# Performance work log

Hardware: AMD Instinct MI355X
Metric: run time of the kernel (lower is better)

Reference implementation:

```python
import jax, jax.numpy as jnp
import numpy as np

N = 10000       # nodes (= number of eigenpairs)
NFEAT = 512
NCLASS = 64     # hidden size of attention/FFN when norm='none'
HID = 128       # feat_encoder hidden
DIM = 32        # eig encoder hidden_dim
K = 10          # outer loop count of ParamNonHarmonicEncoding
NF = DIM // 2   # num_freq = 16
OMEGA = 50.0
DMIN = 0.25
NLAYER = 1


def _ln(x, g, b, eps=1e-5):
    m = jnp.mean(x, axis=-1, keepdims=True)
    v = jnp.mean((x - m) ** 2, axis=-1, keepdims=True)
    return g * (x - m) / jnp.sqrt(v + eps) + b


def setup_inputs() -> dict:
    key = jax.random.key(0)
    ks = jax.random.split(key, 32)
    f32 = jnp.float32
    def w(k, shape, s=0.05):
        return jax.random.normal(k, shape, dtype=f32) * s
    inp = {
        "e": jax.random.uniform(ks[0], (N,), dtype=f32),
        "u": jax.random.normal(ks[1], (N, N), dtype=f32) / np.float32(np.sqrt(N)),
        "x": jax.random.normal(ks[2], (N, NFEAT), dtype=f32),
        # feat_encoder: Linear(nfeat,hid) -> ReLU -> Linear(hid,nclass)
        "fe_w1": w(ks[3], (NFEAT, HID)), "fe_b1": jnp.zeros((HID,), f32),
        "fe_w2": w(ks[4], (HID, NCLASS)), "fe_b2": jnp.zeros((NCLASS,), f32),
        # ParamNonHarmonicEncoding
        "freq_deltas": jax.random.uniform(ks[5], (NF,), dtype=f32) * 0.5,
        "freq_bias": jnp.zeros((), f32),
        "readout_w": w(ks[6], (K, 1 + 2 * NF), 0.1),
        "readout_b": jnp.zeros((K,), f32),
        "alpha_w": w(ks[7], (K, 1), 0.3),   # nn.Linear(k,1,bias=False)
        # mha pre-norm
        "mha_ln_g": jnp.ones((NCLASS,), f32), "mha_ln_b": jnp.zeros((NCLASS,), f32),
        # Diff attention (H=1, hidden=nclass)
        "wq1": w(ks[8], (NCLASS, NCLASS)), "bq1": jnp.zeros((NCLASS,), f32),
        "wk1": w(ks[9], (NCLASS, NCLASS)), "bk1": jnp.zeros((NCLASS,), f32),
        "wq2": w(ks[10], (NCLASS, NCLASS)), "bq2": jnp.zeros((NCLASS,), f32),
        "wk2": w(ks[11], (NCLASS, NCLASS)), "bk2": jnp.zeros((NCLASS,), f32),
        "wv": w(ks[12], (NCLASS, NCLASS)), "bv": jnp.zeros((NCLASS,), f32),
        "lq1": w(ks[13], (NCLASS,), 0.1), "lk1": w(ks[14], (NCLASS,), 0.1),
        "lq2": w(ks[15], (NCLASS,), 0.1), "lk2": w(ks[16], (NCLASS,), 0.1),
        "attn_ln_g": jnp.ones((NCLASS,), f32), "attn_ln_b": jnp.zeros((NCLASS,), f32),
        "out_w": w(ks[17], (NCLASS, NCLASS)), "out_b": jnp.zeros((NCLASS,), f32),
        # gating
        "gate_ln_g": jnp.ones((3 * NCLASS,), f32), "gate_ln_b": jnp.zeros((3 * NCLASS,), f32),
        "gate_w": w(ks[18], (3 * NCLASS, 3)), "gate_b": jnp.zeros((3,), f32),
        # FFN
        "ffn_ln_g": jnp.ones((NCLASS,), f32), "ffn_ln_b": jnp.zeros((NCLASS,), f32),
        "ffn_w1": w(ks[19], (NCLASS, NCLASS)), "ffn_b1": jnp.zeros((NCLASS,), f32),
        "ffn_w2": w(ks[20], (NCLASS, NCLASS)), "ffn_b2": jnp.zeros((NCLASS,), f32),
    }
    return inp


def reference(e, u, x, fe_w1, fe_b1, fe_w2, fe_b2,
              freq_deltas, freq_bias, readout_w, readout_b, alpha_w,
              mha_ln_g, mha_ln_b,
              wq1, bq1, wk1, bk1, wq2, bq2, wk2, bk2, wv, bv,
              lq1, lk1, lq2, lk2, attn_ln_g, attn_ln_b, out_w, out_b,
              gate_ln_g, gate_ln_b, gate_w, gate_b,
              ffn_ln_g, ffn_ln_b, ffn_w1, ffn_b1, ffn_w2, ffn_b2):
    # feat encoder (all dropouts are 0 / eval mode)
    h = jnp.maximum(x @ fe_w1 + fe_b1, 0.0) @ fe_w2 + fe_b2          # [N, C]

    # ParamNonHarmonicEncoding, vectorized over the k powers
    deltas = jax.nn.softplus(freq_deltas) + DMIN
    freqs = jnp.cumsum(deltas) + freq_bias
    freqs = OMEGA * jnp.tanh(freqs / OMEGA)                           # [F]
    powers = e[:, None] ** jnp.arange(1, K + 1, dtype=e.dtype)        # [N, K]
    phase = powers[:, :, None] * freqs                                # [N, K, F]
    ns = jnp.asarray(NF ** 0.5, e.dtype)
    feat = jnp.concatenate(
        [jnp.ones_like(powers)[..., None], jnp.sin(phase) / ns, jnp.cos(phase) / ns],
        axis=-1)                                                      # [N, K, 1+2F]
    eig = jnp.einsum('nkf,kf->nk', feat, readout_w) + readout_b      # [N, K]
    new_e = eig @ alpha_w                                             # [N, 1]

    for layer in range(NLAYER):
        # spectral propagation: u @ diag-like(new_e) @ u^T @ h
        utx = u.T @ h                                                 # [N, C]
        h_fur = u @ (new_e * utx)                                     # [N, C]

        # differential linear attention
        mh = _ln(h, mha_ln_g, mha_ln_b)
        q1 = mh @ wq1 + bq1; k1 = mh @ wk1 + bk1
        q2 = mh @ wq2 + bq2; k2 = mh @ wk2 + bk2
        v = mh @ wv + bv
        k1v = k1.T @ v                                                # [C, C]
        k2v = k2.T @ v
        lam1 = jnp.exp(jnp.sum(lq1 * lk1))
        lam2 = jnp.exp(jnp.sum(lq2 * lk2))
        lam_init = 0.8 - 0.6 * float(np.exp(-0.3 * layer))
        lam_full = lam1 - lam2 + lam_init
        xa = q1 @ k1v - (q2 @ k2v) * lam_full
        xa = _ln(xa, attn_ln_g, attn_ln_b) * (1.0 - lam_init)
        mha_h = xa @ out_w + out_b                                    # [N, C]

        # gated mixing
        cat = jnp.concatenate([h, mha_h, h_fur], axis=-1)             # [N, 3C]
        g = jax.nn.softmax(_ln(cat, gate_ln_g, gate_ln_b) @ gate_w + gate_b, axis=-1)
        mix = h * g[:, 0:1] + mha_h * g[:, 1:2] + h_fur * g[:, 2:3]

        f = _ln(mix, ffn_ln_g, ffn_ln_b)
        f = jax.nn.gelu(f @ ffn_w1 + ffn_b1, approximate=False) @ ffn_w2 + ffn_b2
        h = mix + f
    return h
```

## Files before the change

kernel.cpp:

```cpp
#include <hip/hip_runtime.h>
#include <hip/hip_bf16.h>
#include <math.h>

#define NN 10000
#define J48 10048
#define CHUNKS 157
#define CPS 20
#define SPLITS 8

typedef __bf16 bf16;
typedef bf16 bf16x8 __attribute__((ext_vector_type(8)));
typedef float f32x4 __attribute__((ext_vector_type(4)));

#define SYNC_LDS() do {                                      \
    asm volatile("s_waitcnt lgkmcnt(0)" ::: "memory");       \
    __builtin_amdgcn_sched_barrier(0);                       \
    __builtin_amdgcn_s_barrier();                            \
    __builtin_amdgcn_sched_barrier(0);                       \
  } while (0)

__device__ __forceinline__ float wave_sum64(float v) {
#pragma unroll
  for (int m = 32; m >= 1; m >>= 1) v += __shfl_xor(v, m, 64);
  return v;
}

__global__ void prep_kernel(const float* __restrict__ w1, const float* __restrict__ w2,
                            const float* __restrict__ wq1, const float* __restrict__ wk1,
                            const float* __restrict__ wq2, const float* __restrict__ wk2,
                            const float* __restrict__ wvw,
                            const float* __restrict__ bq1, const float* __restrict__ bk1,
                            const float* __restrict__ bq2, const float* __restrict__ bk2,
                            const float* __restrict__ bvv,
                            const float* __restrict__ lq1, const float* __restrict__ lk1,
                            const float* __restrict__ lq2, const float* __restrict__ lk2,
                            const float* __restrict__ freq_deltas, const float* __restrict__ freq_bias,
                            bf16* __restrict__ w1T, bf16* __restrict__ w2T, bf16* __restrict__ qkvT,
                            float* __restrict__ bqkv, float* __restrict__ freqs, float* __restrict__ lamb) {
  int tid = blockIdx.x * blockDim.x + threadIdx.x;
  int nthr = gridDim.x * blockDim.x;
  for (int i = tid; i < 512 * 128; i += nthr) {
    int o = i >> 9, k = i & 511;
    w1T[i] = (bf16)w1[k * 128 + o];
  }
  for (int i = tid; i < 64 * 128; i += nthr) {
    int o = i >> 7, k = i & 127;
    w2T[i] = (bf16)w2[k * 64 + o];
  }
  for (int i = tid; i < 320 * 64; i += nthr) {
    int r = i >> 6, k = i & 63;
    const float* W = (r < 64) ? wq1 : (r < 128) ? wk1 : (r < 192) ? wq2 : (r < 256) ? wk2 : wvw;
    qkvT[i] = (bf16)W[k * 64 + (r & 63)];
  }
  for (int i = tid; i < 320; i += nthr) {
    const float* B = (i < 64) ? bq1 : (i < 128) ? bk1 : (i < 192) ? bq2 : (i < 256) ? bk2 : bvv;
    bqkv[i] = B[i & 63];
  }
  if (blockIdx.x == 0) {
    if (threadIdx.x == 0) {
      float acc = freq_bias[0];
      for (int f = 0; f < 16; f++) {
        acc += log1pf(expf(freq_deltas[f])) + 0.25f;
        freqs[f] = 50.0f * tanhf(acc * (1.0f / 50.0f));
      }
    }
    if (threadIdx.x >= 64 && threadIdx.x < 128) {
      int l = threadIdx.x - 64;
      float s1 = wave_sum64(lq1[l] * lk1[l]);
      float s2 = wave_sum64(lq2[l] * lk2[l]);
      if (l == 0) lamb[0] = expf(s1) - expf(s2) + 0.2f;
    }
  }
}

__global__ void newe_kernel(const float* __restrict__ e, const float* __restrict__ rw,
                            const float* __restrict__ rb, const float* __restrict__ aw,
                            const float* __restrict__ freqs, float* __restrict__ newe) {
  int n = blockIdx.x * blockDim.x + threadIdx.x;
  if (n >= NN) return;
  float fr[16];
#pragma unroll
  for (int f = 0; f < 16; f++) fr[f] = freqs[f];
  float ev = e[n], p = 1.0f, acc = 0.0f;
  for (int k = 0; k < 10; k++) {
    p *= ev;
    float s = rb[k] + rw[k * 33];
#pragma unroll
    for (int f = 0; f < 16; f++) {
      float ph = p * fr[f];
      s += 0.25f * (__sinf(ph) * rw[k * 33 + 1 + f] + __cosf(ph) * rw[k * 33 + 17 + f]);
    }
    acc += s * aw[k];
  }
  newe[n] = acc;
}

__global__ __launch_bounds__(256) void g1_kernel(const float* __restrict__ x, const bf16* __restrict__ w1T,
                                                 const float* __restrict__ b1, bf16* __restrict__ t1b) {
  __shared__ bf16 la[64][40];
  __shared__ bf16 lb[128][40];
  const int bm = blockIdx.x * 64;
  const int lane = threadIdx.x & 63, wvid = threadIdx.x >> 6;
// ... 138 lines not shown
    uint4 val = make_uint4(0u, 0u, 0u, 0u);
    if (row < NN) val = *(const uint4*)(mh + (size_t)row * 64 + seg);
    *(uint4*)&la[m][seg] = val;
  }
#pragma unroll
  for (int r = 0; r < 10; r++) {
    int slot = threadIdx.x * 10 + r;
    int n = slot >> 3, seg = (slot & 7) * 8;
    *(uint4*)&lb[n][seg] = *(const uint4*)(qkvT + n * 64 + seg);
  }
  __syncthreads();
  f32x4 acc[20] = {};
#pragma unroll
  for (int ks = 0; ks < 2; ks++) {
    bf16x8 af = *(const bf16x8*)&la[wvid * 16 + (lane & 15)][ks * 32 + (lane >> 4) * 8];
#pragma unroll
    for (int s = 0; s < 20; s++) {
      bf16x8 bfr = *(const bf16x8*)&lb[s * 16 + (lane & 15)][ks * 32 + (lane >> 4) * 8];
      acc[s] = __builtin_amdgcn_mfma_f32_16x16x32_bf16(af, bfr, acc[s], 0, 0, 0);
    }
  }
#pragma unroll
  for (int s = 0; s < 20; s++) {
    int col = s * 16 + (lane & 15);
    float bvv = bqkv[col];
    bf16* dst; int dc, stride;
    if (col < 64)       { dst = qq; dc = col;       stride = 128; }
    else if (col < 128) { dst = kv; dc = col - 64;  stride = 192; }
    else if (col < 192) { dst = qq; dc = col - 64;  stride = 128; }
    else                { dst = kv; dc = col - 128; stride = 192; }
#pragma unroll
    for (int r = 0; r < 4; r++) {
      int row = bm + wvid * 16 + (lane >> 4) * 4 + r;
      if (row < NN) dst[(size_t)row * stride + dc] = (bf16)(acc[s][r] + bvv);
    }
  }
}

__global__ __launch_bounds__(256) void r1_kernel(const bf16* __restrict__ kv, float* __restrict__ part) {
  int b = blockIdx.x;
  int c1 = threadIdx.x & 63, grp = threadIdx.x >> 6;
  int r0 = b * 16;
  float a1[16] = {}, a2[16] = {};
  for (int r = 0; r < 16; r++) {
    const bf16* rowp = kv + (size_t)(r0 + r) * 192;
    float k1 = (float)rowp[c1];
    float k2 = (float)rowp[64 + c1];
    union { uint4 v; bf16 b[8]; } v0, v1;
    v0.v = *(const uint4*)(rowp + 128 + grp * 16);
    v1.v = *(const uint4*)(rowp + 136 + grp * 16);
#pragma unroll
    for (int q = 0; q < 8; q++) {
      float va = (float)v0.b[q], vb = (float)v1.b[q];
      a1[q] += k1 * va; a2[q] += k2 * va;
      a1[8 + q] += k1 * vb; a2[8 + q] += k2 * vb;
    }
  }
  float* p1 = part + (size_t)b * 8192 + (size_t)c1 * 64 + grp * 16;
  float* p2 = p1 + 4096;
#pragma unroll
  for (int q = 0; q < 16; q++) { p1[q] = a1[q]; p2[q] = a2[q]; }
}

__global__ __launch_bounds__(256) void r2a_kernel(const float* __restrict__ part, float* __restrict__ part2) {
  int flat = blockIdx.x * 256 + threadIdx.x;
  int y = blockIdx.y;
  int b0 = y * 79, b1 = min(625, b0 + 79);
  float s = 0.f;
  for (int b = b0; b < b1; b++) s += part[(size_t)b * 8192 + flat];
  part2[(size_t)flat * 8 + y] = s;
}

__global__ void r2b_kernel(const float* __restrict__ part2, const float* __restrict__ lamb, bf16* __restrict__ Bt) {
  int flat = blockIdx.x * 256 + threadIdx.x;
  int mat = flat >> 12, rem = flat & 4095;
  int d = rem >> 6, c = rem & 63;
  f32x4 lo = *(const f32x4*)(part2 + (size_t)flat * 8);
  f32x4 hi = *(const f32x4*)(part2 + (size_t)flat * 8 + 4);
  float s = lo[0] + lo[1] + lo[2] + lo[3] + hi[0] + hi[1] + hi[2] + hi[3];
  float v = mat ? (-lamb[0] * s) : s;
  Bt[c * 128 + mat * 64 + d] = (bf16)v;
}

__global__ __launch_bounds__(256) void d_split_kernel(const float* __restrict__ u, const bf16* __restrict__ hT,
                                                      float* __restrict__ dpart) {
  __shared__ bf16 la[64][72];
  __shared__ bf16 lb[64][72];
  const int j0 = blockIdx.x * 64;
  const int sk = blockIdx.y;
  const int c0 = sk * CPS, c1e = min(CHUNKS, c0 + CPS);
  const int t = threadIdx.x;
  const int lane = t & 63, wv = t >> 6;
  const int jl = (t & 15) * 4;
  const int ir = (t >> 4) * 4;
  f32x4 acc[4] = {};
  uint4 aC[2];
  float4 bC[4];
  auto fetchAll = [&](int i0) {
#pragma unroll
    for (int r = 0; r < 2; r++) {
      int slot = t * 2 + r;
      int c = slot >> 3, seg = (slot & 7) * 8;
      int i = i0 + seg;
      if (i + 7 < NN) aC[r] = *(const uint4*)(hT + (size_t)c * NN + i);
      else {
        union { uint4 v; bf16 b[8]; } tu;
#pragma unroll
        for (int q = 0; q < 8; q++) tu.b[q] = (i + q < NN) ? hT[(size_t)c * NN + i + q] : (bf16)0.f;
        aC[r] = tu.v;
      }
    }
#pragma unroll
    for (int q = 0; q < 4; q++) {
      int i = i0 + ir + q;
      if (i < NN && (j0 + jl + 3) < NN) bC[q] = *(const float4*)(u + (size_t)i * NN + j0 + jl);
      else if (i < NN) {
        float tmp[4];
#pragma unroll
        for (int q2 = 0; q2 < 4; q2++) tmp[q2] = (j0 + jl + q2 < NN) ? u[(size_t)i * NN + j0 + jl + q2] : 0.f;
        bC[q] = make_float4(tmp[0], tmp[1], tmp[2], tmp[3]);
      } else bC[q] = make_float4(0.f, 0.f, 0.f, 0.f);
    }
  };
  auto storeAll = [&]() {
#pragma unroll
    for (int r = 0; r < 2; r++) {
      int slot = t * 2 + r;
      int c = slot >> 3, seg = (slot & 7) * 8;
      *(uint4*)&la[c][seg] = aC[r];
    }
#pragma unroll
    for (int q2 = 0; q2 < 4; q2++) {
      int j = jl + q2;
      int isw = ir ^ (((j >> 2) & 3) << 3);
      union { uint2 w; bf16 b[4]; } pk;
      pk.b[0] = (bf16)((float*)&bC[0])[q2];
      pk.b[1] = (bf16)((float*)&bC[1])[q2];
      pk.b[2] = (bf16)((float*)&bC[2])[q2];
      pk.b[3] = (bf16)((float*)&bC[3])[q2];
      *(uint2*)&lb[j][isw] = pk.w;
    }
  };
  fetchAll(c0 * 64);
  for (int ch = c0; ch < c1e; ch++) {
    storeAll();
    if (ch + 1 < c1e) fetchAll((ch + 1) * 64);
    SYNC_LDS();
#pragma unroll
    for (int ks = 0; ks < 2; ks++) {
      bf16x8 af = *(const bf16x8*)&la[wv * 16 + (lane & 15)][ks * 32 + (lane >> 4) * 8];
#pragma unroll
      for (int s = 0; s < 4; s++) {
        int j = s * 16 + (lane & 15);
        int ioff = (ks * 32 + (lane >> 4) * 8) ^ (((j >> 2) & 3) << 3);
        bf16x8 bfr = *(const bf16x8*)&lb[j][ioff];
        acc[s] = __builtin_amdgcn_mfma_f32_16x16x32_bf16(af, bfr, acc[s], 0, 0, 0);
      }
    }
    SYNC_LDS();
  }
#pragma unroll
  for (int s = 0; s < 4; s++) {
    int j = j0 + s * 16 + (lane & 15);
#pragma unroll
    for (int r = 0; r < 4; r++) {
      int c = wv * 16 + (lane >> 4) * 4 + r;
      dpart[((size_t)sk * 64 + c) * J48 + j] = acc[s][r];
    }
  }
}

__global__ void dred_kernel(const float* __restrict__ dpart, const float* __restrict__ newe,
                            bf16* __restrict__ wutxT) {
  int idx = blockIdx.x * 256 + threadIdx.x;
  int c = idx / 2512;
  int j = (idx - c * 2512) * 4;
  if (c >= 64 || j >= NN) return;
  f32x4 s = {};
  for (int sk = 0; sk < SPLITS; sk++)
    s += *(const f32x4*)(dpart + ((size_t)sk * 64 + c) * J48 + j);
  union { uint2 w; bf16 b[4]; } pk;
#pragma unroll
  for (int q = 0; q < 4; q++) pk.b[q] = (bf16)(newe[j + q] * s[q]);
  *(uint2*)&wutxT[(size_t)c * NN + j] = pk.w;
}

__global__ __launch_bounds__(256) void e_split_kernel(const float* __restrict__ u, const bf16* __restrict__ wutxT,
                                                      float* __restrict__ epart) {
  __shared__ bf16 la[64][72];
  __shared__ bf16 lb[64][72];
  const int bm = blockIdx.x * 64;
  const int sk = blockIdx.y;
  const int c0 = sk * CPS, c1e = min(CHUNKS, c0 + CPS);
  const int t = threadIdx.x;
  const int lane = t & 63, wv = t >> 6;
  const int mA = t >> 2, segA = (t & 3) * 16;
  const int mrow = bm + mA;
  f32x4 acc[4] = {};
  float4 aC[4];
  uint4 bC[2];
  auto fetchAll = [&](int j0) {
    int j = j0 + segA;
    if (mrow < NN && j + 15 < NN) {
      const float4* p = (const float4*)(u + (size_t)mrow * NN + j);
      aC[0] = p[0]; aC[1] = p[1]; aC[2] = p[2]; aC[3] = p[3];
    } else {
#pragma unroll
      for (int q = 0; q < 4; q++) {
        float tmp[4];
#pragma unroll
        for (int q2 = 0; q2 < 4; q2++) {
          int jj = j + q * 4 + q2;
          tmp[q2] = (mrow < NN && jj < NN) ? u[(size_t)mrow * NN + jj] : 0.f;
        }
        aC[q] = make_float4(tmp[0], tmp[1], tmp[2], tmp[3]);
      }
    }
#pragma unroll
    for (int r = 0; r < 2; r++) {
      int slot = t * 2 + r;
      int c = slot >> 3, seg = (slot & 7) * 8;
      int jj = j0 + seg;
      if (jj + 7 < NN) bC[r] = *(const uint4*)(wutxT + (size_t)c * NN + jj);
      else {
        union { uint4 v; bf16 b[8]; } tu;
#pragma unroll
        for (int q = 0; q < 8; q++) tu.b[q] = (jj + q < NN) ? wutxT[(size_t)c * NN + jj + q] : (bf16)0.f;
        bC[r] = tu.v;
      }
    }
  };
  auto storeAll = [&]() {
    union { uint4 v[2]; bf16 b[16]; } pk;
#pragma unroll
    for (int q = 0; q < 4; q++)
#pragma unroll
      for (int q2 = 0; q2 < 4; q2++) pk.b[q * 4 + q2] = (bf16)((float*)&aC[q])[q2];
    *(uint4*)&la[mA][segA] = pk.v[0];
    *(uint4*)&la[mA][segA + 8] = pk.v[1];
#pragma unroll
    for (int r = 0; r < 2; r++) {
      int slot = t * 2 + r;
      int c = slot >> 3, seg = (slot & 7) * 8;
      *(uint4*)&lb[c][seg] = bC[r];
    }
  };
  fetchAll(c0 * 64);
  for (int ch = c0; ch < c1e; ch++) {
    storeAll();
    if (ch + 1 < c1e) fetchAll((ch + 1) * 64);
    SYNC_LDS();
#pragma unroll
    for (int ks = 0; ks < 2; ks++) {
      bf16x8 af = *(const bf16x8*)&la[wv * 16 + (lane & 15)][ks * 32 + (lane >> 4) * 8];
#pragma unroll
      for (int s = 0; s < 4; s++) {
        bf16x8 bfr = *(const bf16x8*)&lb[s * 16 + (lane & 15)][ks * 32 + (lane >> 4) * 8];
        acc[s] = __builtin_amdgcn_mfma_f32_16x16x32_bf16(af, bfr, acc[s], 0, 0, 0);
      }
    }
    SYNC_LDS();
  }
#pragma unroll
  for (int s = 0; s < 4; s++) {
    int col = s * 16 + (lane & 15);
#pragma unroll
    for (int r = 0; r < 4; r++) {
      int row = wv * 16 + (lane >> 4) * 4 + r;
      epart[((size_t)sk * J48 + bm + row) * 64 + col] = acc[s][r];
    }
  }
}

__global__ void ered_kernel(const float* __restrict__ epart, float* __restrict__ h_fur) {
  int idx = blockIdx.x * 256 + threadIdx.x;
  if (idx >= NN * 16) return;
  size_t off = (size_t)idx * 4;
  f32x4 s = {};
  for (int sk = 0; sk < SPLITS; sk++)
    s += *(const f32x4*)(epart + (size_t)sk * (J48 * 64) + off);
  *(f32x4*)(h_fur + off) = s;
}

__global__ __launch_bounds__(256) void hattn_kernel(const bf16* __restrict__ qq, const bf16* __restrict__ Bt,
                                                    const float* __restrict__ g, const float* __restrict__ b,
                                                    bf16* __restrict__ xan) {
  __shared__ bf16 la[64][136];
  __shared__ bf16 lb[64][136];
  const int bm = blockIdx.x * 64;
  const int lane = threadIdx.x & 63, wvid = threadIdx.x >> 6;
#pragma unroll
  for (int r = 0; r < 4; r++) {
    int slot = threadIdx.x * 4 + r;
    int m = slot >> 4, seg = (slot & 15) * 8;
    int row = bm + m;
    uint4 val = make_uint4(0u, 0u, 0u, 0u);
    if (row < NN) val = *(const uint4*)(qq + (size_t)row * 128 + seg);
    *(uint4*)&la[m][seg] = val;
    *(uint4*)&lb[m][seg] = *(const uint4*)(Bt + m * 128 + seg);
  }
  __syncthreads();
  f32x4 acc[4] = {};
#pragma unroll
  for (int ks = 0; ks < 4; ks++) {
    bf16x8 af = *(const bf16x8*)&la[wvid * 16 + (lane & 15)][ks * 32 + (lane >> 4) * 8];
#pragma unroll
    for (int s = 0; s < 4; s++) {
      bf16x8 bfr = *(const bf16x8*)&lb[s * 16 + (lane & 15)][ks * 32 + (lane >> 4) * 8];
      acc[s] = __builtin_amdgcn_mfma_f32_16x16x32_bf16(af, bfr, acc[s], 0, 0, 0);
    }
  }
#pragma unroll
  for (int r = 0; r < 4; r++) {
    float psum = acc[0][r] + acc[1][r] + acc[2][r] + acc[3][r];
#pragma unroll
    for (int msk = 1; msk < 16; msk <<= 1) psum += __shfl_xor(psum, msk, 64);
    float mean = psum * (1.0f / 64.0f);
    float pvar = 0.f;
#pragma unroll
    for (int s = 0; s < 4; s++) { float dd = acc[s][r] - mean; pvar += dd * dd; }
#pragma unroll
    for (int msk = 1; msk < 16; msk <<= 1) pvar += __shfl_xor(pvar, msk, 64);
    float rsq = rsqrtf(pvar * (1.0f / 64.0f) + 1e-5f);
    int row = bm + wvid * 16 + (lane >> 4) * 4 + r;
    if (row < NN) {
#pragma unroll
      for (int s = 0; s < 4; s++) {
        int col = s * 16 + (lane & 15);
        float o = 0.8f * (g[col] * (acc[s][r] - mean) * rsq + b[col]);
        xan[(size_t)row * 64 + col] = (bf16)o;
      }
    }
  }
}

__global__ __launch_bounds__(256) void final_kernel(const float* __restrict__ h, const float* __restrict__ h_fur,
                                                    const bf16* __restrict__ xan,
                                                    const float* __restrict__ out_w, const float* __restrict__ out_b,
                                                    const float* __restrict__ gg, const float* __restrict__ gb,
                                                    const float* __restrict__ gw, const float* __restrict__ gbias,
                                                    const float* __restrict__ fg, const float* __restrict__ fb,
                                                    const float* __restrict__ fw1, const float* __restrict__ fb1,
                                                    const float* __restrict__ fw2, const float* __restrict__ fb2,
                                                    float* __restrict__ out) {
  __shared__ float s_ow[64][64];
  __shared__ float s_w1[64][64];
  __shared__ float s_w2[64][64];
  __shared__ float s_gw[192][3];
  __shared__ float s_row[4][64];
  const int lane = threadIdx.x & 63, wvid = threadIdx.x >> 6;
  for (int i = threadIdx.x; i < 4096; i += 256) {
    ((float*)s_ow)[i] = out_w[i];
    ((float*)s_w1)[i] = fw1[i];
    ((float*)s_w2)[i] = fw2[i];
  }
  for (int i = threadIdx.x; i < 576; i += 256) ((float*)s_gw)[i] = gw[i];
  const int row = blockIdx.x * 4 + wvid;
  float x_h = h[(size_t)row * 64 + lane];
  float x_f = h_fur[(size_t)row * 64 + lane];
  float x_a = (float)xan[(size_t)row * 64 + lane];
  s_row[wvid][lane] = x_a;
  __syncthreads();
  float mha = out_b[lane];
#pragma unroll 8
  for (int d = 0; d < 64; d++) mha += s_row[wvid][d] * s_ow[d][lane];
  float m3 = wave_sum64(x_h + mha + x_f) * (1.0f / 192.0f);
  float dh = x_h - m3, dm = mha - m3, df = x_f - m3;
  float v3 = wave_sum64(dh * dh + dm * dm + df * df) * (1.0f / 192.0f);
  float rs3 = rsqrtf(v3 + 1e-5f);
  float l0 = gg[lane] * dh * rs3 + gb[lane];
  float l1 = gg[64 + lane] * dm * rs3 + gb[64 + lane];
  float l2 = gg[128 + lane] * df * rs3 + gb[128 + lane];
  float p0 = l0 * s_gw[lane][0] + l1 * s_gw[64 + lane][0] + l2 * s_gw[128 + lane][0];
  float p1 = l0 * s_gw[lane][1] + l1 * s_gw[64 + lane][1] + l2 * s_gw[128 + lane][1];
  float p2 = l0 * s_gw[lane][2] + l1 * s_gw[64 + lane][2] + l2 * s_gw[128 + lane][2];
  p0 = wave_sum64(p0) + gbias[0];
  p1 = wave_sum64(p1) + gbias[1];
  p2 = wave_sum64(p2) + gbias[2];
  float mx = fmaxf(p0, fmaxf(p1, p2));
  float e0 = expf(p0 - mx), e1 = expf(p1 - mx), e2 = expf(p2 - mx);
  float inv = 1.0f / (e0 + e1 + e2);
  float mix = x_h * (e0 * inv) + mha * (e1 * inv) + x_f * (e2 * inv);
  float mf = wave_sum64(mix) * (1.0f / 64.0f);
  float dmx = mix - mf;
  float vf = wave_sum64(dmx * dmx) * (1.0f / 64.0f);
  float f = fg[lane] * dmx * rsqrtf(vf + 1e-5f) + fb[lane];
  __syncthreads();
  s_row[wvid][lane] = f;
  __syncthreads();
  float t1 = fb1[lane];
#pragma unroll 8
  for (int d = 0; d < 64; d++) t1 += s_row[wvid][d] * s_w1[d][lane];
  t1 = 0.5f * t1 * (1.0f + erff(t1 * 0.70710678118654752f));
  __syncthreads();
  s_row[wvid][lane] = t1;
  __syncthreads();
  float f2 = fb2[lane];
#pragma unroll 8
  for (int d = 0; d < 64; d++) f2 += s_row[wvid][d] * s_w2[d][lane];
  out[(size_t)row * 64 + lane] = mix + f2;
}

extern "C" void kernel_launch(void* const* d_in, const int* in_sizes, int n_in,
                              void* d_out, int out_size, void* d_ws, size_t ws_size,
                              hipStream_t stream) {
  const float* e          = (const float*)d_in[0];
  const float* u          = (const float*)d_in[1];
  const float* x          = (const float*)d_in[2];
  const float* fe_w1      = (const float*)d_in[3];
  const float* fe_b1      = (const float*)d_in[4];
  const float* fe_w2      = (const float*)d_in[5];
  const float* fe_b2      = (const float*)d_in[6];
  const float* freq_deltas= (const float*)d_in[7];
  const float* freq_bias  = (const float*)d_in[8];
  const float* readout_w  = (const float*)d_in[9];
  const float* readout_b  = (const float*)d_in[10];
  const float* alpha_w    = (const float*)d_in[11];
  const float* mha_ln_g   = (const float*)d_in[12];
  const float* mha_ln_b   = (const float*)d_in[13];
  const float* wq1        = (const float*)d_in[14];
  const float* bq1        = (const float*)d_in[15];
  const float* wk1        = (const float*)d_in[16];
  const float* bk1        = (const float*)d_in[17];
  const float* wq2        = (const float*)d_in[18];
  const float* bq2        = (const float*)d_in[19];
  const float* wk2        = (const float*)d_in[20];
  const float* bk2        = (const float*)d_in[21];
  const float* wv_in      = (const float*)d_in[22];
  const float* bv_in      = (const float*)d_in[23];
  const float* lq1        = (const float*)d_in[24];
  const float* lk1        = (const float*)d_in[25];
  const float* lq2        = (const float*)d_in[26];
  const float* lk2        = (const float*)d_in[27];
  const float* attn_ln_g  = (const float*)d_in[28];
  const float* attn_ln_b  = (const float*)d_in[29];
  const float* out_w      = (const float*)d_in[30];
  const float* out_b      = (const float*)d_in[31];
  const float* gate_ln_g  = (const float*)d_in[32];
  const float* gate_ln_b  = (const float*)d_in[33];
  const float* gate_w     = (const float*)d_in[34];
  const float* gate_b     = (const float*)d_in[35];
  const float* ffn_ln_g   = (const float*)d_in[36];
  const float* ffn_ln_b   = (const float*)d_in[37];
  const float* ffn_w1     = (const float*)d_in[38];
  const float* ffn_b1     = (const float*)d_in[39];
  const float* ffn_w2     = (const float*)d_in[40];
  const float* ffn_b2     = (const float*)d_in[41];

  constexpr size_t OFF_H     = 0;
  constexpr size_t OFF_T1B   = 2560000;
  constexpr size_t OFF_HT    = 5120000;
  constexpr size_t OFF_MH    = 6400000;
  constexpr size_t OFF_QQ    = 7680000;
  constexpr size_t OFF_KV    = 10240000;
  constexpr size_t OFF_WUTXT = 14080000;
  constexpr size_t OFF_HFUR  = 15360000;
  constexpr size_t OFF_XAN   = 17920000;
  constexpr size_t OFF_NEWE  = 19200000;
  constexpr size_t OFF_BT    = 19240064;
  constexpr size_t OFF_W1T   = 19256448;
  constexpr size_t OFF_W2T   = 19387520;
  constexpr size_t OFF_QKVT  = 19403904;
  constexpr size_t OFF_BQKV  = 19444864;
  constexpr size_t OFF_FREQS = 19446144;
  constexpr size_t OFF_LAM   = 19446208;
  constexpr size_t OFF_BIG   = 19446272;
  constexpr size_t SZ_SPART  = (size_t)SPLITS * 64 * J48 * 4;
  constexpr size_t OFF_PART2 = OFF_BIG + SZ_SPART;
  constexpr size_t WS_NEED   = OFF_PART2 + 262144;
  if (ws_size < WS_NEED) return;

  char* ws = (char*)d_ws;
  float* h_buf   = (float*)(ws + OFF_H);
  bf16*  t1b     = (bf16*)(ws + OFF_T1B);
  bf16*  hT      = (bf16*)(ws + OFF_HT);
  bf16*  mh      = (bf16*)(ws + OFF_MH);
  bf16*  qq      = (bf16*)(ws + OFF_QQ);
  bf16*  kv      = (bf16*)(ws + OFF_KV);
  bf16*  wutxT   = (bf16*)(ws + OFF_WUTXT);
  float* h_fur   = (float*)(ws + OFF_HFUR);
  bf16*  xan     = (bf16*)(ws + OFF_XAN);
  float* newe    = (float*)(ws + OFF_NEWE);
  bf16*  Bt      = (bf16*)(ws + OFF_BT);
  bf16*  w1T     = (bf16*)(ws + OFF_W1T);
  bf16*  w2T     = (bf16*)(ws + OFF_W2T);
  bf16*  qkvT    = (bf16*)(ws + OFF_QKVT);
  float* bqkv    = (float*)(ws + OFF_BQKV);
  float* freqs   = (float*)(ws + OFF_FREQS);
  float* lamb    = (float*)(ws + OFF_LAM);
  float* part    = (float*)(ws + OFF_BIG);
  float* part2   = (float*)(ws + OFF_PART2);
  float* dpart   = (float*)(ws + OFF_BIG);
  float* epart   = (float*)(ws + OFF_BIG);

  prep_kernel<<<64, 256, 0, stream>>>(fe_w1, fe_w2, wq1, wk1, wq2, wk2, wv_in,
                                      bq1, bk1, bq2, bk2, bv_in,
                                      lq1, lk1, lq2, lk2, freq_deltas, freq_bias,
                                      w1T, w2T, qkvT, bqkv, freqs, lamb);
  newe_kernel<<<40, 256, 0, stream>>>(e, readout_w, readout_b, alpha_w, freqs, newe);
  g1_kernel<<<157, 256, 0, stream>>>(x, w1T, fe_b1, t1b);
  g2_kernel<<<157, 256, 0, stream>>>(t1b, w2T, fe_b2, mha_ln_g, mha_ln_b, h_buf, hT, mh);
  qkv_kernel<<<157, 256, 0, stream>>>(mh, qkvT, bqkv, qq, kv);
  r1_kernel<<<625, 256, 0, stream>>>(kv, part);
  r2a_kernel<<<dim3(32, 8), 256, 0, stream>>>(part, part2);
  r2b_kernel<<<32, 256, 0, stream>>>(part2, lamb, Bt);
  d_split_kernel<<<dim3(157, SPLITS), 256, 0, stream>>>(u, hT, dpart);
  dred_kernel<<<628, 256, 0, stream>>>(dpart, newe, wutxT);
  e_split_kernel<<<dim3(157, SPLITS), 256, 0, stream>>>(u, wutxT, epart);
  ered_kernel<<<625, 256, 0, stream>>>(epart, h_fur);
  hattn_kernel<<<157, 256, 0, stream>>>(qq, Bt, attn_ln_g, attn_ln_b, xan);
  final_kernel<<<2500, 256, 0, stream>>>(h_buf, h_fur, xan, out_w, out_b,
                                         gate_ln_g, gate_ln_b, gate_w, gate_b,
                                         ffn_ln_g, ffn_ln_b, ffn_w1, ffn_b1, ffn_w2, ffn_b2,
                                         (float*)d_out);
}
```

Baseline: 361.1 us.

## Retile U-transpose and U matmuls with wider tiles and full-row u loads

Rewrites the two large GEMMs over the 10000x10000 u matrix. The u^T·h kernel now computes 64x256 output tiles with 16 MFMA accumulators per wave across 16 K-splits, using a new two-level swizzle. The u·(new_e·utx) kernel now loads 256-column u strips per chunk with XOR swizzling and walks K in four 64-wide inner steps. Both aim at better memory coalescing of the streamed u and fewer wasted edge tiles. The register double-buffered prefetch is removed in favour of plain __syncthreads, which risks exposing global-load latency.

```diff
diff --git a/kernel.cpp b/kernel.cpp
--- a/kernel.cpp
+++ b/kernel.cpp
@@ -5,19 +5,14 @@
 #define NN 10000
 #define J48 10048
 #define CHUNKS 157
-#define CPS 20
-#define SPLITS 8
+#define DJP 10240
+#define DSK 16
+#define DCPS 10
+#define ESK 8
 
 typedef __bf16 bf16;
 typedef bf16 bf16x8 __attribute__((ext_vector_type(8)));
 typedef float f32x4 __attribute__((ext_vector_type(4)));
-
-#define SYNC_LDS() do {                                      \
-    asm volatile("s_waitcnt lgkmcnt(0)" ::: "memory");       \
-    __builtin_amdgcn_sched_barrier(0);                       \
-    __builtin_amdgcn_s_barrier();                            \
-    __builtin_amdgcn_sched_barrier(0);                       \
-  } while (0)
 
 __device__ __forceinline__ float wave_sum64(float v) {
 #pragma unroll
@@ -322,184 +317,171 @@
   Bt[c * 128 + mat * 64 + d] = (bf16)v;
 }
 
-__global__ __launch_bounds__(256) void d_split_kernel(const float* __restrict__ u, const bf16* __restrict__ hT,
-                                                      float* __restrict__ dpart) {
+__global__ __launch_bounds__(256) void d4_kernel(const float* __restrict__ u, const bf16* __restrict__ hT,
+                                                 float* __restrict__ dpart) {
   __shared__ bf16 la[64][72];
-  __shared__ bf16 lb[64][72];
-  const int j0 = blockIdx.x * 64;
+  __shared__ bf16 lb[256][72];
+  const int j0 = blockIdx.x * 256;
   const int sk = blockIdx.y;
-  const int c0 = sk * CPS, c1e = min(CHUNKS, c0 + CPS);
+  const int c0 = sk * DCPS, c1e = min(CHUNKS, c0 + DCPS);
   const int t = threadIdx.x;
   const int lane = t & 63, wv = t >> 6;
-  const int jl = (t & 15) * 4;
-  const int ir = (t >> 4) * 4;
-  f32x4 acc[4] = {};
-  uint4 aC[2];
-  float4 bC[4];
-  auto fetchAll = [&](int i0) {
+  const int jl = (t & 63) * 4;
+  f32x4 acc[4][4] = {};
+  for (int ch = c0; ch < c1e; ch++) {
+    const int i0 = ch * 64;
 #pragma unroll
     for (int r = 0; r < 2; r++) {
       int slot = t * 2 + r;
       int c = slot >> 3, seg = (slot & 7) * 8;
       int i = i0 + seg;
-      if (i + 7 < NN) aC[r] = *(const uint4*)(hT + (size_t)c * NN + i);
+      uint4 v;
+      if (i + 7 < NN) v = *(const uint4*)(hT + (size_t)c * NN + i);
       else {
         union { uint4 v; bf16 b[8]; } tu;
 #pragma unroll
         for (int q = 0; q < 8; q++) tu.b[q] = (i + q < NN) ? hT[(size_t)c * NN + i + q] : (bf16)0.f;
-        aC[r] = tu.v;
-      }
-    }
-#pragma unroll
-    for (int q = 0; q < 4; q++) {
-      int i = i0 + ir + q;
-      if (i < NN && (j0 + jl + 3) < NN) bC[q] = *(const float4*)(u + (size_t)i * NN + j0 + jl);
-      else if (i < NN) {
-        float tmp[4];
-#pragma unroll
-        for (int q2 = 0; q2 < 4; q2++) tmp[q2] = (j0 + jl + q2 < NN) ? u[(size_t)i * NN + j0 + jl + q2] : 0.f;
-        bC[q] = make_float4(tmp[0], tmp[1], tmp[2], tmp[3]);
-      } else bC[q] = make_float4(0.f, 0.f, 0.f, 0.f);
-    }
-  };
-  auto storeAll = [&]() {
-#pragma unroll
-    for (int r = 0; r < 2; r++) {
-      int slot = t * 2 + r;
-      int c = slot >> 3, seg = (slot & 7) * 8;
-      *(uint4*)&la[c][seg] = aC[r];
-    }
-#pragma unroll
-    for (int q2 = 0; q2 < 4; q2++) {
-      int j = jl + q2;
-      int isw = ir ^ (((j >> 2) & 3) << 3);
-      union { uint2 w; bf16 b[4]; } pk;
-      pk.b[0] = (bf16)((float*)&bC[0])[q2];
-      pk.b[1] = (bf16)((float*)&bC[1])[q2];
-      pk.b[2] = (bf16)((float*)&bC[2])[q2];
-      pk.b[3] = (bf16)((float*)&bC[3])[q2];
-      *(uint2*)&lb[j][isw] = pk.w;
-    }
-  };
-  fetchAll(c0 * 64);
-  for (int ch = c0; ch < c1e; ch++) {
-    storeAll();
-    if (ch + 1 < c1e) fetchAll((ch + 1) * 64);
-    SYNC_LDS();
+        v = tu.v;
+      }
+      *(uint4*)&la[c][seg] = v;
+    }
+#pragma unroll
+    for (int e = 0; e < 4; e++) {
+      float4 bC[4];
+      const int ib = e * 16 + wv * 4;
+#pragma unroll
+      for (int q = 0; q < 4; q++) {
+        int i = i0 + ib + q;
+        int j = j0 + jl;
+        if (i < NN && j + 3 < NN) bC[q] = *(const float4*)(u + (size_t)i * NN + j);
+        else if (i < NN) {
+          float tmp[4];
+#pragma unroll
+          for (int q2 = 0; q2 < 4; q2++) tmp[q2] = (j + q2 < NN) ? u[(size_t)i * NN + j + q2] : 0.f;
+          bC[q] = make_float4(tmp[0], tmp[1], tmp[2], tmp[3]);
+        } else bC[q] = make_float4(0.f, 0.f, 0.f, 0.f);
+      }
+#pragma unroll
+      for (int q2 = 0; q2 < 4; q2++) {
+        int j = jl + q2;
+        int swz = ((j >> 2) ^ (j >> 5)) & 7;
+        int iw = ib ^ (swz << 3);
+        union { uint w[2]; bf16 b[4]; } pk;
+        pk.b[0] = (bf16)((const float*)&bC[0])[q2];
+        pk.b[1] = (bf16)((const float*)&bC[1])[q2];
+        pk.b[2] = (bf16)((const float*)&bC[2])[q2];
+        pk.b[3] = (bf16)((const float*)&bC[3])[q2];
+        *(uint2*)&lb[j][iw] = *(const uint2*)pk.w;
+      }
+    }
+    __syncthreads();
 #pragma unroll
     for (int ks = 0; ks < 2; ks++) {
-      bf16x8 af = *(const bf16x8*)&la[wv * 16 + (lane & 15)][ks * 32 + (lane >> 4) * 8];
-#pragma unroll
-      for (int s = 0; s < 4; s++) {
-        int j = s * 16 + (lane & 15);
-        int ioff = (ks * 32 + (lane >> 4) * 8) ^ (((j >> 2) & 3) << 3);
+      bf16x8 af[4];
+#pragma unroll
+      for (int m = 0; m < 4; m++)
+        af[m] = *(const bf16x8*)&la[m * 16 + (lane & 15)][ks * 32 + (lane >> 4) * 8];
+#pragma unroll
+      for (int n = 0; n < 4; n++) {
+        int j = wv * 64 + n * 16 + (lane & 15);
+        int swz = ((j >> 2) ^ (j >> 5)) & 7;
+        int ioff = (ks * 32 + (lane >> 4) * 8) ^ (swz << 3);
         bf16x8 bfr = *(const bf16x8*)&lb[j][ioff];
-        acc[s] = __builtin_amdgcn_mfma_f32_16x16x32_bf16(af, bfr, acc[s], 0, 0, 0);
-      }
-    }
-    SYNC_LDS();
-  }
-#pragma unroll
-  for (int s = 0; s < 4; s++) {
-    int j = j0 + s * 16 + (lane & 15);
-#pragma unroll
-    for (int r = 0; r < 4; r++) {
-      int c = wv * 16 + (lane >> 4) * 4 + r;
-      dpart[((size_t)sk * 64 + c) * J48 + j] = acc[s][r];
-    }
-  }
+#pragma unroll
+        for (int m = 0; m < 4; m++)
+          acc[m][n] = __builtin_amdgcn_mfma_f32_16x16x32_bf16(af[m], bfr, acc[m][n], 0, 0, 0);
+      }
+    }
+    __syncthreads();
+  }
+#pragma unroll
+  for (int m = 0; m < 4; m++)
+#pragma unroll
+    for (int n = 0; n < 4; n++) {
+      int j = j0 + wv * 64 + n * 16 + (lane & 15);
+#pragma unroll
+      for (int r = 0; r < 4; r++) {
+        int c = m * 16 + (lane >> 4) * 4 + r;
+        dpart[((size_t)sk * 64 + c) * DJP + j] = acc[m][n][r];
+      }
+    }
 }
 
 __global__ void dred_kernel(const float* __restrict__ dpart, const float* __restrict__ newe,
                             bf16* __restrict__ wutxT) {
   int idx = blockIdx.x * 256 + threadIdx.x;
-  int c = idx / 2512;
-  int j = (idx - c * 2512) * 4;
-  if (c >= 64 || j >= NN) return;
+  int c = idx / 2500;
+  int j = (idx - c * 2500) * 4;
+  if (c >= 64) return;
   f32x4 s = {};
-  for (int sk = 0; sk < SPLITS; sk++)
-    s += *(const f32x4*)(dpart + ((size_t)sk * 64 + c) * J48 + j);
+  for (int sk = 0; sk < DSK; sk++)
+    s += *(const f32x4*)(dpart + ((size_t)sk * 64 + c) * DJP + j);
   union { uint2 w; bf16 b[4]; } pk;
 #pragma unroll
   for (int q = 0; q < 4; q++) pk.b[q] = (bf16)(newe[j + q] * s[q]);
   *(uint2*)&wutxT[(size_t)c * NN + j] = pk.w;
 }
 
-__global__ __launch_bounds__(256) void e_split_kernel(const float* __restrict__ u, const bf16* __restrict__ wutxT,
-                                                      float* __restrict__ epart) {
-  __shared__ bf16 la[64][72];
+__global__ __launch_bounds__(256) void e4_kernel(const float* __restrict__ u, const bf16* __restrict__ wutxT,
+                                                 float* __restrict__ epart) {
+  __shared__ bf16 la[64][264];
   __shared__ bf16 lb[64][72];
   const int bm = blockIdx.x * 64;
   const int sk = blockIdx.y;
-  const int c0 = sk * CPS, c1e = min(CHUNKS, c0 + CPS);
   const int t = threadIdx.x;
   const int lane = t & 63, wv = t >> 6;
-  const int mA = t >> 2, segA = (t & 3) * 16;
-  const int mrow = bm + mA;
+  const int jl = (t & 63) * 4;
   f32x4 acc[4] = {};
-  float4 aC[4];
-  uint4 bC[2];
-  auto fetchAll = [&](int j0) {
-    int j = j0 + segA;
-    if (mrow < NN && j + 15 < NN) {
-      const float4* p = (const float4*)(u + (size_t)mrow * NN + j);
-      aC[0] = p[0]; aC[1] = p[1]; aC[2] = p[2]; aC[3] = p[3];
-    } else {
-#pragma unroll
-      for (int q = 0; q < 4; q++) {
+  for (int cj = sk * 5; cj < sk * 5 + 5; cj++) {
+    const int jg0 = cj * 256;
+#pragma unroll
+    for (int is = 0; is < 16; is++) {
+      int il = is * 4 + wv;
+      int i = bm + il;
+      int j = jg0 + jl;
+      float4 v;
+      if (i < NN && j + 3 < NN) v = *(const float4*)(u + (size_t)i * NN + j);
+      else if (i < NN) {
         float tmp[4];
 #pragma unroll
-        for (int q2 = 0; q2 < 4; q2++) {
-          int jj = j + q * 4 + q2;
-          tmp[q2] = (mrow < NN && jj < NN) ? u[(size_t)mrow * NN + jj] : 0.f;
+        for (int q2 = 0; q2 < 4; q2++) tmp[q2] = (j + q2 < NN) ? u[(size_t)i * NN + j + q2] : 0.f;
+        v = make_float4(tmp[0], tmp[1], tmp[2], tmp[3]);
+      } else v = make_float4(0.f, 0.f, 0.f, 0.f);
+      union { uint w[2]; bf16 b[4]; } pk;
+      pk.b[0] = (bf16)v.x; pk.b[1] = (bf16)v.y; pk.b[2] = (bf16)v.z; pk.b[3] = (bf16)v.w;
+      *(uint2*)&la[il][jl ^ ((il & 7) << 3)] = *(const uint2*)pk.w;
+    }
+#pragma unroll
+    for (int inner = 0; inner < 4; inner++) {
+#pragma unroll
+      for (int r = 0; r < 2; r++) {
+        int slot = t * 2 + r;
+        int c = slot >> 3, seg = (slot & 7) * 8;
+        int jj = jg0 + inner * 64 + seg;
+        uint4 v;
+        if (jj + 7 < NN) v = *(const uint4*)(wutxT + (size_t)c * NN + jj);
+        else {
+          union { uint4 v; bf16 b[8]; } tu;
+#pragma unroll
+          for (int q = 0; q < 8; q++) tu.b[q] = (jj + q < NN) ? wutxT[(size_t)c * NN + jj + q] : (bf16)0.f;
+          v = tu.v;
         }
-        aC[q] = make_float4(tmp[0], tmp[1], tmp[2], tmp[3]);
-      }
-    }
-#pragma unroll
-    for (int r = 0; r < 2; r++) {
-      int slot = t * 2 + r;
-      int c = slot >> 3, seg = (slot & 7) * 8;
-      int jj = j0 + seg;
-      if (jj + 7 < NN) bC[r] = *(const uint4*)(wutxT + (size_t)c * NN + jj);
-      else {
-        union { uint4 v; bf16 b[8]; } tu;
-#pragma unroll
-        for (int q = 0; q < 8; q++) tu.b[q] = (jj + q < NN) ? wutxT[(size_t)c * NN + jj + q] : (bf16)0.f;
-        bC[r] = tu.v;
-      }
-    }
-  };
-  auto storeAll = [&]() {
-    union { uint4 v[2]; bf16 b[16]; } pk;
-#pragma unroll
-    for (int q = 0; q < 4; q++)
-#pragma unroll
-      for (int q2 = 0; q2 < 4; q2++) pk.b[q * 4 + q2] = (bf16)((float*)&aC[q])[q2];
-    *(uint4*)&la[mA][segA] = pk.v[0];
-    *(uint4*)&la[mA][segA + 8] = pk.v[1];
-#pragma unroll
-    for (int r = 0; r < 2; r++) {
-      int slot = t * 2 + r;
-      int c = slot >> 3, seg = (slot & 7) * 8;
-      *(uint4*)&lb[c][seg] = bC[r];
-    }
-  };
-  fetchAll(c0 * 64);
-  for (int ch = c0; ch < c1e; ch++) {
-    storeAll();
-    if (ch + 1 < c1e) fetchAll((ch + 1) * 64);
-    SYNC_LDS();
-#pragma unroll
-    for (int ks = 0; ks < 2; ks++) {
-      bf16x8 af = *(const bf16x8*)&la[wv * 16 + (lane & 15)][ks * 32 + (lane >> 4) * 8];
-#pragma unroll
-      for (int s = 0; s < 4; s++) {
-        bf16x8 bfr = *(const bf16x8*)&lb[s * 16 + (lane & 15)][ks * 32 + (lane >> 4) * 8];
-        acc[s] = __builtin_amdgcn_mfma_f32_16x16x32_bf16(af, bfr, acc[s], 0, 0, 0);
-      }
-    }
-    SYNC_LDS();
+        *(uint4*)&lb[c][seg] = v;
+      }
+      __syncthreads();
+#pragma unroll
+      for (int ks = 0; ks < 2; ks++) {
+        int il = wv * 16 + (lane & 15);
+        int joff = (inner * 64 + ks * 32 + (lane >> 4) * 8) ^ ((il & 7) << 3);
+        bf16x8 af = *(const bf16x8*)&la[il][joff];
+#pragma unroll
+        for (int s = 0; s < 4; s++) {
+          bf16x8 bfr = *(const bf16x8*)&lb[s * 16 + (lane & 15)][ks * 32 + (lane >> 4) * 8];
+          acc[s] = __builtin_amdgcn_mfma_f32_16x16x32_bf16(af, bfr, acc[s], 0, 0, 0);
+        }
+      }
+      __syncthreads();
+    }
   }
 #pragma unroll
   for (int s = 0; s < 4; s++) {
@@ -517,7 +499,7 @@
   if (idx >= NN * 16) return;
   size_t off = (size_t)idx * 4;
   f32x4 s = {};
-  for (int sk = 0; sk < SPLITS; sk++)
+  for (int sk = 0; sk < ESK; sk++)
     s += *(const f32x4*)(epart + (size_t)sk * (J48 * 64) + off);
   *(f32x4*)(h_fur + off) = s;
 }
@@ -705,8 +687,8 @@
   constexpr size_t OFF_FREQS = 19446144;
   constexpr size_t OFF_LAM   = 19446208;
   constexpr size_t OFF_BIG   = 19446272;
-  constexpr size_t SZ_SPART  = (size_t)SPLITS * 64 * J48 * 4;
-  constexpr size_t OFF_PART2 = OFF_BIG + SZ_SPART;
+  constexpr size_t SZ_DPART  = (size_t)DSK * 64 * DJP * 4;
+  constexpr size_t OFF_PART2 = OFF_BIG + SZ_DPART;
   constexpr size_t WS_NEED   = OFF_PART2 + 262144;
   if (ws_size < WS_NEED) return;
 
@@ -744,9 +726,9 @@
   r1_kernel<<<625, 256, 0, stream>>>(kv, part);
   r2a_kernel<<<dim3(32, 8), 256, 0, stream>>>(part, part2);
   r2b_kernel<<<32, 256, 0, stream>>>(part2, lamb, Bt);
-  d_split_kernel<<<dim3(157, SPLITS), 256, 0, stream>>>(u, hT, dpart);
-  dred_kernel<<<628, 256, 0, stream>>>(dpart, newe, wutxT);
-  e_split_kernel<<<dim3(157, SPLITS), 256, 0, stream>>>(u, wutxT, epart);
+  d4_kernel<<<dim3(40, DSK), 256, 0, stream>>>(u, hT, dpart);
+  dred_kernel<<<625, 256, 0, stream>>>(dpart, newe, wutxT);
+  e4_kernel<<<dim3(157, ESK), 256, 0, stream>>>(u, wutxT, epart);
   ered_kernel<<<625, 256, 0, stream>>>(epart, h_fur);
   hattn_kernel<<<157, 256, 0, stream>>>(qq, Bt, attn_ln_g, attn_ln_b, xan);
   final_kernel<<<2500, 256, 0, stream>>>(h_buf, h_fur, xan, out_w, out_b,
```

Result: slower. 430.0 us (+19.1%).

## Widen u^T·h tile to 256 columns, resplit K, fuse e-reduction into final

Applied to the files above, without the earlier changes.

The u^T h GEMM kernel now computes a 64x256 output tile per block, with each wave holding a 4x4 grid of MFMA accumulators. The K dimension is split into 20 parts of 8 chunks each, and the LDS B tile uses a new XOR swizzle. Each A fragment is now reused across more columns, and the 40x20 grid is meant to spread the u stream evenly across CUs. The separate ered reduction kernel is removed and the final kernel sums the 8 epart slices directly. The custom LDS sync macro is replaced by __syncthreads. In exchange the split-K partial buffer grows, dred must read more partials, and register pressure is higher.

```diff
diff --git a/kernel.cpp b/kernel.cpp
--- a/kernel.cpp
+++ b/kernel.cpp
@@ -6,18 +6,14 @@
 #define J48 10048
 #define CHUNKS 157
 #define CPS 20
-#define SPLITS 8
+#define ESPLITS 8
+#define DJP 10240
+#define DSPLITS 20
+#define DCPS 8
 
 typedef __bf16 bf16;
 typedef bf16 bf16x8 __attribute__((ext_vector_type(8)));
 typedef float f32x4 __attribute__((ext_vector_type(4)));
-
-#define SYNC_LDS() do {                                      \
-    asm volatile("s_waitcnt lgkmcnt(0)" ::: "memory");       \
-    __builtin_amdgcn_sched_barrier(0);                       \
-    __builtin_amdgcn_s_barrier();                            \
-    __builtin_amdgcn_sched_barrier(0);                       \
-  } while (0)
 
 __device__ __forceinline__ float wave_sum64(float v) {
 #pragma unroll
@@ -322,44 +318,58 @@
   Bt[c * 128 + mat * 64 + d] = (bf16)v;
 }
 
-__global__ __launch_bounds__(256) void d_split_kernel(const float* __restrict__ u, const bf16* __restrict__ hT,
-                                                      float* __restrict__ dpart) {
+__global__ __launch_bounds__(256) void d5_kernel(const float* __restrict__ u, const bf16* __restrict__ hT,
+                                                 float* __restrict__ dpart) {
   __shared__ bf16 la[64][72];
-  __shared__ bf16 lb[64][72];
-  const int j0 = blockIdx.x * 64;
+  __shared__ bf16 lb[256][72];
+  const int j0 = blockIdx.x * 256;
   const int sk = blockIdx.y;
-  const int c0 = sk * CPS, c1e = min(CHUNKS, c0 + CPS);
+  const int c0 = sk * DCPS, c1e = min(CHUNKS, c0 + DCPS);
   const int t = threadIdx.x;
   const int lane = t & 63, wv = t >> 6;
-  const int jl = (t & 15) * 4;
-  const int ir = (t >> 4) * 4;
-  f32x4 acc[4] = {};
-  uint4 aC[2];
-  float4 bC[4];
+  const int jl = lane * 4;
+  f32x4 acc[4][4] = {};
+  uint4 hA[2];
+  uint2 upk[4][4];
   auto fetchAll = [&](int i0) {
 #pragma unroll
     for (int r = 0; r < 2; r++) {
       int slot = t * 2 + r;
       int c = slot >> 3, seg = (slot & 7) * 8;
       int i = i0 + seg;
-      if (i + 7 < NN) aC[r] = *(const uint4*)(hT + (size_t)c * NN + i);
+      if (i + 7 < NN) hA[r] = *(const uint4*)(hT + (size_t)c * NN + i);
       else {
         union { uint4 v; bf16 b[8]; } tu;
 #pragma unroll
         for (int q = 0; q < 8; q++) tu.b[q] = (i + q < NN) ? hT[(size_t)c * NN + i + q] : (bf16)0.f;
-        aC[r] = tu.v;
-      }
-    }
-#pragma unroll
-    for (int q = 0; q < 4; q++) {
-      int i = i0 + ir + q;
-      if (i < NN && (j0 + jl + 3) < NN) bC[q] = *(const float4*)(u + (size_t)i * NN + j0 + jl);
-      else if (i < NN) {
-        float tmp[4];
-#pragma unroll
-        for (int q2 = 0; q2 < 4; q2++) tmp[q2] = (j0 + jl + q2 < NN) ? u[(size_t)i * NN + j0 + jl + q2] : 0.f;
-        bC[q] = make_float4(tmp[0], tmp[1], tmp[2], tmp[3]);
-      } else bC[q] = make_float4(0.f, 0.f, 0.f, 0.f);
+        hA[r] = tu.v;
+      }
+    }
+    int j = j0 + jl;
+#pragma unroll
+    for (int e = 0; e < 4; e++) {
+      float4 bC[4];
+      int rb = i0 + e * 16 + wv * 4;
+#pragma unroll
+      for (int q = 0; q < 4; q++) {
+        int i = rb + q;
+        if (i < NN && j + 3 < NN) bC[q] = *(const float4*)(u + (size_t)i * NN + j);
+        else if (i < NN) {
+          float tmp[4];
+#pragma unroll
+          for (int q2 = 0; q2 < 4; q2++) tmp[q2] = (j + q2 < NN) ? u[(size_t)i * NN + j + q2] : 0.f;
+          bC[q] = make_float4(tmp[0], tmp[1], tmp[2], tmp[3]);
+        } else bC[q] = make_float4(0.f, 0.f, 0.f, 0.f);
+      }
+#pragma unroll
+      for (int q2 = 0; q2 < 4; q2++) {
+        union { uint2 w; bf16 b[4]; } pk;
+        pk.b[0] = (bf16)((const float*)&bC[0])[q2];
+        pk.b[1] = (bf16)((const float*)&bC[1])[q2];
+        pk.b[2] = (bf16)((const float*)&bC[2])[q2];
+        pk.b[3] = (bf16)((const float*)&bC[3])[q2];
+        upk[e][q2] = pk.w;
+      }
     }
   };
   auto storeAll = [&]() {
@@ -367,58 +377,65 @@
     for (int r = 0; r < 2; r++) {
       int slot = t * 2 + r;
       int c = slot >> 3, seg = (slot & 7) * 8;
-      *(uint4*)&la[c][seg] = aC[r];
-    }
-#pragma unroll
-    for (int q2 = 0; q2 < 4; q2++) {
-      int j = jl + q2;
-      int isw = ir ^ (((j >> 2) & 3) << 3);
-      union { uint2 w; bf16 b[4]; } pk;
-      pk.b[0] = (bf16)((float*)&bC[0])[q2];
-      pk.b[1] = (bf16)((float*)&bC[1])[q2];
-      pk.b[2] = (bf16)((float*)&bC[2])[q2];
-      pk.b[3] = (bf16)((float*)&bC[3])[q2];
-      *(uint2*)&lb[j][isw] = pk.w;
+      *(uint4*)&la[c][seg] = hA[r];
+    }
+#pragma unroll
+    for (int e = 0; e < 4; e++) {
+      int ib = e * 16 + wv * 4;
+#pragma unroll
+      for (int q2 = 0; q2 < 4; q2++) {
+        int j = jl + q2;
+        int swz = ((j >> 2) ^ (j >> 5)) & 7;
+        *(uint2*)&lb[j][ib ^ (swz << 3)] = upk[e][q2];
+      }
     }
   };
   fetchAll(c0 * 64);
   for (int ch = c0; ch < c1e; ch++) {
     storeAll();
     if (ch + 1 < c1e) fetchAll((ch + 1) * 64);
-    SYNC_LDS();
+    __syncthreads();
 #pragma unroll
     for (int ks = 0; ks < 2; ks++) {
-      bf16x8 af = *(const bf16x8*)&la[wv * 16 + (lane & 15)][ks * 32 + (lane >> 4) * 8];
-#pragma unroll
-      for (int s = 0; s < 4; s++) {
-        int j = s * 16 + (lane & 15);
-        int ioff = (ks * 32 + (lane >> 4) * 8) ^ (((j >> 2) & 3) << 3);
+      bf16x8 af[4];
+#pragma unroll
+      for (int m = 0; m < 4; m++)
+        af[m] = *(const bf16x8*)&la[m * 16 + (lane & 15)][ks * 32 + (lane >> 4) * 8];
+#pragma unroll
+      for (int n = 0; n < 4; n++) {
+        int j = wv * 64 + n * 16 + (lane & 15);
+        int swz = ((j >> 2) ^ (j >> 5)) & 7;
+        int ioff = (ks * 32 + (lane >> 4) * 8) ^ (swz << 3);
         bf16x8 bfr = *(const bf16x8*)&lb[j][ioff];
-        acc[s] = __builtin_amdgcn_mfma_f32_16x16x32_bf16(af, bfr, acc[s], 0, 0, 0);
-      }
-    }
-    SYNC_LDS();
-  }
-#pragma unroll
-  for (int s = 0; s < 4; s++) {
-    int j = j0 + s * 16 + (lane & 15);
-#pragma unroll
-    for (int r = 0; r < 4; r++) {
-      int c = wv * 16 + (lane >> 4) * 4 + r;
-      dpart[((size_t)sk * 64 + c) * J48 + j] = acc[s][r];
-    }
-  }
+#pragma unroll
+        for (int m = 0; m < 4; m++)
+          acc[m][n] = __builtin_amdgcn_mfma_f32_16x16x32_bf16(af[m], bfr, acc[m][n], 0, 0, 0);
+      }
+    }
+    __syncthreads();
+  }
+#pragma unroll
+  for (int m = 0; m < 4; m++)
+#pragma unroll
+    for (int n = 0; n < 4; n++) {
+      int j = j0 + wv * 64 + n * 16 + (lane & 15);
+#pragma unroll
+      for (int r = 0; r < 4; r++) {
+        int c = m * 16 + (lane >> 4) * 4 + r;
+        dpart[((size_t)sk * 64 + c) * DJP + j] = acc[m][n][r];
+      }
+    }
 }
 
 __global__ void dred_kernel(const float* __restrict__ dpart, const float* __restrict__ newe,
                             bf16* __restrict__ wutxT) {
   int idx = blockIdx.x * 256 + threadIdx.x;
-  int c = idx / 2512;
-  int j = (idx - c * 2512) * 4;
+  int c = idx / 2560;
+  int j = (idx - c * 2560) * 4;
   if (c >= 64 || j >= NN) return;
   f32x4 s = {};
-  for (int sk = 0; sk < SPLITS; sk++)
-    s += *(const f32x4*)(dpart + ((size_t)sk * 64 + c) * J48 + j);
+  for (int sk = 0; sk < DSPLITS; sk++)
+    s += *(const f32x4*)(dpart + ((size_t)sk * 64 + c) * DJP + j);
   union { uint2 w; bf16 b[4]; } pk;
 #pragma unroll
   for (int q = 0; q < 4; q++) pk.b[q] = (bf16)(newe[j + q] * s[q]);
@@ -489,7 +506,7 @@
   for (int ch = c0; ch < c1e; ch++) {
     storeAll();
     if (ch + 1 < c1e) fetchAll((ch + 1) * 64);
-    SYNC_LDS();
+    __syncthreads();
 #pragma unroll
     for (int ks = 0; ks < 2; ks++) {
       bf16x8 af = *(const bf16x8*)&la[wv * 16 + (lane & 15)][ks * 32 + (lane >> 4) * 8];
@@ -499,7 +516,7 @@
         acc[s] = __builtin_amdgcn_mfma_f32_16x16x32_bf16(af, bfr, acc[s], 0, 0, 0);
       }
     }
-    SYNC_LDS();
+    __syncthreads();
   }
 #pragma unroll
   for (int s = 0; s < 4; s++) {
@@ -510,16 +527,6 @@
       epart[((size_t)sk * J48 + bm + row) * 64 + col] = acc[s][r];
     }
   }
-}
-
-__global__ void ered_kernel(const float* __restrict__ epart, float* __restrict__ h_fur) {
-  int idx = blockIdx.x * 256 + threadIdx.x;
-  if (idx >= NN * 16) return;
-  size_t off = (size_t)idx * 4;
-  f32x4 s = {};
-  for (int sk = 0; sk < SPLITS; sk++)
-    s += *(const f32x4*)(epart + (size_t)sk * (J48 * 64) + off);
-  *(f32x4*)(h_fur + off) = s;
 }
 
 __global__ __launch_bounds__(256) void hattn_kernel(const bf16* __restrict__ qq, const bf16* __restrict__ Bt,
@@ -574,7 +581,7 @@
   }
 }
 
-__global__ __launch_bounds__(256) void final_kernel(const float* __restrict__ h, const float* __restrict__ h_fur,
+__global__ __launch_bounds__(256) void final_kernel(const float* __restrict__ h, const float* __restrict__ epart,
                                                     const bf16* __restrict__ xan,
                                                     const float* __restrict__ out_w, const float* __restrict__ out_b,
                                                     const float* __restrict__ gg, const float* __restrict__ gb,
@@ -597,7 +604,10 @@
   for (int i = threadIdx.x; i < 576; i += 256) ((float*)s_gw)[i] = gw[i];
   const int row = blockIdx.x * 4 + wvid;
   float x_h = h[(size_t)row * 64 + lane];
-  float x_f = h_fur[(size_t)row * 64 + lane];
+  float x_f = 0.f;
+#pragma unroll
+  for (int sk = 0; sk < ESPLITS; sk++)
+    x_f += epart[((size_t)sk * J48 + row) * 64 + lane];
   float x_a = (float)xan[(size_t)row * 64 + lane];
   s_row[wvid][lane] = x_a;
   __syncthreads();
@@ -705,8 +715,8 @@
   constexpr size_t OFF_FREQS = 19446144;
   constexpr size_t OFF_LAM   = 19446208;
   constexpr size_t OFF_BIG   = 19446272;
-  constexpr size_t SZ_SPART  = (size_t)SPLITS * 64 * J48 * 4;
-  constexpr size_t OFF_PART2 = OFF_BIG + SZ_SPART;
+  constexpr size_t SZ_DPART  = (size_t)DSPLITS * 64 * DJP * 4;
+  constexpr size_t OFF_PART2 = OFF_BIG + SZ_DPART;
   constexpr size_t WS_NEED   = OFF_PART2 + 262144;
   if (ws_size < WS_NEED) return;
 
@@ -718,7 +728,6 @@
   bf16*  qq      = (bf16*)(ws + OFF_QQ);
   bf16*  kv      = (bf16*)(ws + OFF_KV);
   bf16*  wutxT   = (bf16*)(ws + OFF_WUTXT);
-  float* h_fur   = (float*)(ws + OFF_HFUR);
   bf16*  xan     = (bf16*)(ws + OFF_XAN);
   float* newe    = (float*)(ws + OFF_NEWE);
   bf16*  Bt      = (bf16*)(ws + OFF_BT);
@@ -744,12 +753,11 @@
   r1_kernel<<<625, 256, 0, stream>>>(kv, part);
   r2a_kernel<<<dim3(32, 8), 256, 0, stream>>>(part, part2);
   r2b_kernel<<<32, 256, 0, stream>>>(part2, lamb, Bt);
-  d_split_kernel<<<dim3(157, SPLITS), 256, 0, stream>>>(u, hT, dpart);
-  dred_kernel<<<628, 256, 0, stream>>>(dpart, newe, wutxT);
-  e_split_kernel<<<dim3(157, SPLITS), 256, 0, stream>>>(u, wutxT, epart);
-  ered_kernel<<<625, 256, 0, stream>>>(epart, h_fur);
+  d5_kernel<<<dim3(40, DSPLITS), 256, 0, stream>>>(u, hT, dpart);
+  dred_kernel<<<640, 256, 0, stream>>>(dpart, newe, wutxT);
+  e_split_kernel<<<dim3(157, ESPLITS), 256, 0, stream>>>(u, wutxT, epart);
   hattn_kernel<<<157, 256, 0, stream>>>(qq, Bt, attn_ln_g, attn_ln_b, xan);
-  final_kernel<<<2500, 256, 0, stream>>>(h_buf, h_fur, xan, out_w, out_b,
+  final_kernel<<<2500, 256, 0, stream>>>(h_buf, epart, xan, out_w, out_b,
                                          gate_ln_g, gate_ln_b, gate_w, gate_b,
                                          ffn_ln_g, ffn_ln_b, ffn_w1, ffn_b1, ffn_w2, ffn_b2,
                                          (float*)d_out);
```

New measurement: 447.7 us. 1.24x slower.
